# Performance work log

Hardware: AMD Instinct MI355X
Metric: run time of the kernel (lower is better)

## Reference

```python
import jax, jax.numpy as jnp
import numpy as np


def _build_tree(N: int, n: int, seed: int = 0):
    """Random forest encoded as parent pointers + sibling ranks.

    parents:  int32 [N+1]; parents[i] in [0, i) for i>0, root(0) and sentinel(N) -> N.
    child_pos: int32 [N+1]; rank among siblings (in_edges order); >= n means the
               one-hot code is all zeros (matches torch.eye rows beyond n, and roots).
    """
    rng = np.random.default_rng(seed)
    parents = np.empty(N + 1, dtype=np.int32)
    parents[0] = N                      # root -> sentinel
    parents[1:N] = rng.integers(0, np.arange(1, N))  # parent of i is an earlier node
    parents[N] = N                      # sentinel self-loop

    pa = parents[:N].astype(np.int64)
    order = np.argsort(pa, kind="stable")
    sorted_pa = pa[order]
    _, first_idx, inv = np.unique(sorted_pa, return_index=True, return_inverse=True)
    rank = np.arange(N) - first_idx[inv]           # sibling rank within each parent group
    child_pos = np.empty(N + 1, dtype=np.int32)
    child_pos[order] = rank.astype(np.int32)
    child_pos[0] = n                    # root has no parent -> zero code
    child_pos[N] = n                    # sentinel -> zero code
    return parents, child_pos


def setup_inputs() -> dict:
    N, n, k = 262144, 32, 16
    parents, child_pos = _build_tree(N, n)
    return {
        "parents": jnp.asarray(parents),
        "child_pos": jnp.asarray(child_pos),
        "n": n,
        "k": k,
    }


def reference(parents, child_pos, n, k):
    """pos_embeds[node] = concat_{t=0..k-1} onehot(child_pos(ancestor_t(node)), n).

    This is the closed form of the original layer-by-layer scatter:
      pos[child, :n]  = eye row (sibling rank one-hot)
      pos[child, n:]  = pos[parent, :-n]
    Roots keep all-zero codes (child_pos = n -> out-of-range one-hot = zeros).
    """
    N = parents.shape[0] - 1

    def step(cur, _):
        code = jax.nn.one_hot(child_pos[cur], n, dtype=jnp.float32)  # [N, n]
        return parents[cur], code

    _, codes = jax.lax.scan(step, jnp.arange(N, dtype=parents.dtype), None, length=k)
    # codes: [k, N, n] -> [N, k*n] with slot 0 (own code) first
    return jnp.transpose(codes, (1, 0, 2)).reshape(N, k * n)
```

## Files before the change

kernel.cpp:

```cpp
#include <hip/hip_runtime.h>


#define NN 32
#define KK 16
#define NPB 256

__global__ __launch_bounds__(256) void pe_merge(
    const int* __restrict__ parents,
    const int* __restrict__ child_pos,
    int2* __restrict__ comb, int Np1)
{
    const int i = blockIdx.x * 256 + threadIdx.x;
    if (i < Np1) comb[i] = make_int2(parents[i], child_pos[i]);
}

__global__ __launch_bounds__(256, 8) void pe_fused(
    const int2* __restrict__ comb,
    float* __restrict__ out, int N)
{
    __shared__ unsigned char codes[NPB * KK];

    const int tid   = threadIdx.x;
    const int node0 = blockIdx.x * NPB;
    const int node  = node0 + tid;

    unsigned int packed[KK / 4];
    if (node < N) {
        int cur = node;
        #pragma unroll
        for (int w = 0; w < KK / 4; ++w) {
            unsigned int u = 0;
            #pragma unroll
            for (int b = 0; b < 4; ++b) {
                const int2 pc = comb[cur];
                const unsigned int byte =
                    (pc.y < NN) ? (unsigned int)pc.y : 0xFFu;
                u |= byte << (8 * b);
                cur = pc.x;
            }
            packed[w] = u;
        }
    } else {
        #pragma unroll
        for (int w = 0; w < KK / 4; ++w) packed[w] = 0xFFFFFFFFu;
    }
    *reinterpret_cast<uint4*>(&codes[tid * KK]) =
        make_uint4(packed[0], packed[1], packed[2], packed[3]);
    __syncthreads();

    const int t_seg = (tid >> 3) & 15;
    const int q4    = (tid & 7) * 4;
    const int hi    = tid >> 7;
    float4* out4 = reinterpret_cast<float4*>(out) + (size_t)node0 * (NN * KK / 4);

    #pragma unroll 4
    for (int iter = 0; iter < (NPB * KK * NN / 4) / 256; ++iter) {
        const int nl   = 2 * iter + hi;
        const int code = codes[nl * KK + t_seg];
        float4 v;
        v.x = (code == q4    ) ? 1.0f : 0.0f;
        v.y = (code == q4 + 1) ? 1.0f : 0.0f;
        v.z = (code == q4 + 2) ? 1.0f : 0.0f;
        v.w = (code == q4 + 3) ? 1.0f : 0.0f;
        if (node0 + nl < N)
            out4[(size_t)iter * 256 + tid] = v;
    }
}

__global__ __launch_bounds__(256, 8) void pe_kernel(
    const int* __restrict__ parents,
    const int* __restrict__ child_pos,
    float* __restrict__ out, int N)
{
    __shared__ unsigned char codes[NPB * KK];
    const int tid   = threadIdx.x;
    const int node0 = blockIdx.x * NPB;
    const int node  = node0 + tid;

    unsigned int packed[KK / 4];
    if (node < N) {
        int cur = node;
        #pragma unroll
        for (int w = 0; w < KK / 4; ++w) {
            unsigned int u = 0;
            #pragma unroll
            for (int b = 0; b < 4; ++b) {
                int cp = child_pos[cur];
                unsigned int byte = (cp < NN) ? (unsigned int)cp : 0xFFu;
                u |= byte << (8 * b);
                cur = parents[cur];
            }
            packed[w] = u;
        }
    } else {
        #pragma unroll
        for (int w = 0; w < KK / 4; ++w) packed[w] = 0xFFFFFFFFu;
    }
    *reinterpret_cast<uint4*>(&codes[tid * KK]) =
        make_uint4(packed[0], packed[1], packed[2], packed[3]);
    __syncthreads();

    const int t_seg = (tid >> 3) & 15;
    const int q4    = (tid & 7) * 4;
    const int hi    = tid >> 7;
    float4* out4 = reinterpret_cast<float4*>(out) + (size_t)node0 * (NN * KK / 4);

    #pragma unroll 4
    for (int iter = 0; iter < (NPB * KK * NN / 4) / 256; ++iter) {
        const int nl   = 2 * iter + hi;
        const int code = codes[nl * KK + t_seg];
        float4 v;
        v.x = (code == q4    ) ? 1.0f : 0.0f;
        v.y = (code == q4 + 1) ? 1.0f : 0.0f;
        v.z = (code == q4 + 2) ? 1.0f : 0.0f;
        v.w = (code == q4 + 3) ? 1.0f : 0.0f;
        if (node0 + nl < N)
            out4[(size_t)iter * 256 + tid] = v;
    }
}

extern "C" void kernel_launch(void* const* d_in, const int* in_sizes, int n_in,
                              void* d_out, int out_size, void* d_ws, size_t ws_size,
                              hipStream_t stream) {
    const int* parents   = (const int*)d_in[0];
    const int* child_pos = (const int*)d_in[1];
    float* out = (float*)d_out;

    const int N   = in_sizes[0] - 1;
    const int Np1 = N + 1;

    if (ws_size >= (size_t)Np1 * sizeof(int2)) {
        pe_merge<<<(Np1 + 255) / 256, 256, 0, stream>>>(
            parents, child_pos, (int2*)d_ws, Np1);
        pe_fused<<<(N + NPB - 1) / NPB, 256, 0, stream>>>(
            (const int2*)d_ws, out, N);
    } else {
        pe_kernel<<<(N + NPB - 1) / NPB, 256, 0, stream>>>(
            parents, child_pos, out, N);
    }
}
```

Baseline: 113.6 us.

## Split ancestor walk and one-hot expansion into separate kernels with grid-stride writer

```diff
diff --git a/kernel.cpp b/kernel.cpp
--- a/kernel.cpp
+++ b/kernel.cpp
@@ -4,6 +4,8 @@
 #define NN 32
 #define KK 16
 #define NPB 256
+
+typedef float f32x4 __attribute__((ext_vector_type(4)));
 
 __global__ __launch_bounds__(256) void pe_merge(
     const int* __restrict__ parents,
@@ -14,56 +16,50 @@
     if (i < Np1) comb[i] = make_int2(parents[i], child_pos[i]);
 }
 
-__global__ __launch_bounds__(256, 8) void pe_fused(
+__global__ __launch_bounds__(256) void pe_codes(
     const int2* __restrict__ comb,
-    float* __restrict__ out, int N)
+    uint4* __restrict__ codes_out, int N)
 {
-    __shared__ unsigned char codes[NPB * KK];
+    const int node = blockIdx.x * blockDim.x + threadIdx.x;
+    if (node >= N) return;
+    unsigned int packed[KK / 4];
+    int cur = node;
+    #pragma unroll
+    for (int w = 0; w < KK / 4; ++w) {
+        unsigned int u = 0;
+        #pragma unroll
+        for (int b = 0; b < 4; ++b) {
+            const int2 pc = comb[cur];
+            const unsigned int byte = (pc.y < NN) ? (unsigned int)pc.y : 0xFFu;
+            u |= byte << (8 * b);
+            cur = pc.x;
+        }
+        packed[w] = u;
+    }
+    codes_out[node] = make_uint4(packed[0], packed[1], packed[2], packed[3]);
+}
 
-    const int tid   = threadIdx.x;
-    const int node0 = blockIdx.x * NPB;
-    const int node  = node0 + tid;
-
-    unsigned int packed[KK / 4];
-    if (node < N) {
-        int cur = node;
-        #pragma unroll
-        for (int w = 0; w < KK / 4; ++w) {
-            unsigned int u = 0;
-            #pragma unroll
-            for (int b = 0; b < 4; ++b) {
-                const int2 pc = comb[cur];
-                const unsigned int byte =
-                    (pc.y < NN) ? (unsigned int)pc.y : 0xFFu;
-                u |= byte << (8 * b);
-                cur = pc.x;
-            }
-            packed[w] = u;
-        }
-    } else {
-        #pragma unroll
-        for (int w = 0; w < KK / 4; ++w) packed[w] = 0xFFFFFFFFu;
-    }
-    *reinterpret_cast<uint4*>(&codes[tid * KK]) =
-        make_uint4(packed[0], packed[1], packed[2], packed[3]);
-    __syncthreads();
-
-    const int t_seg = (tid >> 3) & 15;
-    const int q4    = (tid & 7) * 4;
-    const int hi    = tid >> 7;
-    float4* out4 = reinterpret_cast<float4*>(out) + (size_t)node0 * (NN * KK / 4);
+__global__ __launch_bounds__(256) void pe_expand_s(
+    const unsigned long long* __restrict__ codes8,
+    f32x4* __restrict__ out4, int total_hr)
+{
+    const int lane = threadIdx.x & 63;
+    const int wid  = (int)((blockIdx.x * blockDim.x + threadIdx.x) >> 6);
+    const int nw   = (int)((gridDim.x * blockDim.x) >> 6);
+    const int tl8  = (lane >> 3) * 8;
+    const int q4   = (lane & 7) * 4;
 
     #pragma unroll 4
-    for (int iter = 0; iter < (NPB * KK * NN / 4) / 256; ++iter) {
-        const int nl   = 2 * iter + hi;
-        const int code = codes[nl * KK + t_seg];
-        float4 v;
+    for (int hr = wid; hr < total_hr; hr += nw) {
+        const int hr_s = __builtin_amdgcn_readfirstlane(hr);
+        const unsigned long long c8 = codes8[hr_s];
+        const int code = (int)((c8 >> tl8) & 0xFFu);
+        f32x4 v;
         v.x = (code == q4    ) ? 1.0f : 0.0f;
         v.y = (code == q4 + 1) ? 1.0f : 0.0f;
         v.z = (code == q4 + 2) ? 1.0f : 0.0f;
         v.w = (code == q4 + 3) ? 1.0f : 0.0f;
-        if (node0 + nl < N)
-            out4[(size_t)iter * 256 + tid] = v;
+        out4[(size_t)hr_s * 64 + lane] = v;
     }
 }
 
@@ -129,11 +125,22 @@
     const int N   = in_sizes[0] - 1;
     const int Np1 = N + 1;
 
-    if (ws_size >= (size_t)Np1 * sizeof(int2)) {
+    const size_t comb_bytes  = (size_t)Np1 * sizeof(int2);
+    const size_t codes_off   = (comb_bytes + 15) & ~(size_t)15;
+    const size_t need        = codes_off + (size_t)N * KK;
+
+    if (ws_size >= need) {
+        char* ws = (char*)d_ws;
+        int2* comb   = (int2*)ws;
+        uint4* codes = (uint4*)(ws + codes_off);
+
         pe_merge<<<(Np1 + 255) / 256, 256, 0, stream>>>(
-            parents, child_pos, (int2*)d_ws, Np1);
-        pe_fused<<<(N + NPB - 1) / NPB, 256, 0, stream>>>(
-            (const int2*)d_ws, out, N);
+            parents, child_pos, comb, Np1);
+        pe_codes<<<(N + 255) / 256, 256, 0, stream>>>(comb, codes, N);
+
+        const int total_hr = N * 2;
+        pe_expand_s<<<1024, 256, 0, stream>>>(
+            (const unsigned long long*)codes, (f32x4*)out, total_hr);
     } else {
         pe_kernel<<<(N + NPB - 1) / NPB, 256, 0, stream>>>(
             parents, child_pos, out, N);
```

New measurement: 146.6 us. 29.0% more time.
